# Kernel tuning notes

Hardware: AMD Instinct MI355X
Metric: run time of the kernel (lower is better)

## Reference

```python
import jax, jax.numpy as jnp
import numpy as np

B, STATE_DIM, REF_DIM, T, H, ACT_DIM = 2048, 32, 16, 100, 256, 2
IN_DIM = STATE_DIM + REF_DIM  # 48


def setup_inputs() -> dict:
    key = jax.random.key(0)
    ks = jax.random.split(key, 12)
    s = 1.0 / np.sqrt(H)  # PyTorch GRU init scale
    obs = jax.random.normal(ks[0], (B, STATE_DIM + T * REF_DIM), jnp.float32)
    u = lambda k, shape: jax.random.uniform(k, shape, jnp.float32, -s, s)
    return {
        "obs": obs,
        "w_ih_l0": u(ks[1], (3 * H, IN_DIM)),
        "w_hh_l0": u(ks[2], (3 * H, H)),
        "b_ih_l0": u(ks[3], (3 * H,)),
        "b_hh_l0": u(ks[4], (3 * H,)),
        "w_ih_l1": u(ks[5], (3 * H, H)),
        "w_hh_l1": u(ks[6], (3 * H, H)),
        "b_ih_l1": u(ks[7], (3 * H,)),
        "b_hh_l1": u(ks[8], (3 * H,)),
        "fc_w": u(ks[9], (ACT_DIM, H)),
        "fc_b": u(ks[10], (ACT_DIM,)),
        "act_high": jnp.ones((ACT_DIM,), jnp.float32),
        "act_low": -jnp.ones((ACT_DIM,), jnp.float32),
    }


def _gru_layer(x, w_ih, w_hh, b_ih, b_hh):
    # x: [B, T, D] -> outputs [B, T, H]; PyTorch GRU gate math (r, z, n order)
    h_dim = w_hh.shape[1]
    xg = jnp.einsum("btd,gd->btg", x, w_ih) + b_ih  # [B, T, 3H], precompute input gates

    def step(h, xg_t):
        hg = h @ w_hh.T + b_hh
        xr, xz, xn = jnp.split(xg_t, 3, axis=-1)
        hr, hz, hn = jnp.split(hg, 3, axis=-1)
        r = jax.nn.sigmoid(xr + hr)
        z = jax.nn.sigmoid(xz + hz)
        n = jnp.tanh(xn + r * hn)
        h_new = (1.0 - z) * n + z * h
        return h_new, h_new

    h0 = jnp.zeros((x.shape[0], h_dim), x.dtype)
    _, hs = jax.lax.scan(step, h0, jnp.swapaxes(xg, 0, 1))  # [T, B, H]
    return jnp.swapaxes(hs, 0, 1)


def reference(obs, w_ih_l0, w_hh_l0, b_ih_l0, b_hh_l0, w_ih_l1, w_hh_l1, b_ih_l1, b_hh_l1, fc_w, fc_b, act_high, act_low):
    state = obs[:, :STATE_DIM]                                  # [B, S]
    traj = obs[:, STATE_DIM:].reshape(obs.shape[0], -1, REF_DIM)  # [B, T, R]
    seq_len = traj.shape[1]
    state_exp = jnp.broadcast_to(state[:, None, :], (obs.shape[0], seq_len, STATE_DIM))
    x = jnp.concatenate([state_exp, traj], axis=2)              # [B, T, S+R]
    out = _gru_layer(x, w_ih_l0, w_hh_l0, b_ih_l0, b_hh_l0)
    out = _gru_layer(out, w_ih_l1, w_hh_l1, b_ih_l1, b_hh_l1)
    last = out[:, -1, :]                                        # [B, H]
    actions = last @ fc_w.T + fc_b                              # [B, A]
    return (act_high - act_low) / 2 * jnp.tanh(actions) + (act_high + act_low) / 2
```

## Files before the change

kernel.cpp:

```cpp
#include <hip/hip_runtime.h>
#include <hip/hip_bf16.h>
#include <stdint.h>
#include <stddef.h>


#define OBS_STRIDE 1632
#define H 256
#define M 16
#define THREADS 512

typedef __attribute__((ext_vector_type(8))) short bfrag8;
typedef __attribute__((ext_vector_type(4))) short bfrag4;
typedef __attribute__((ext_vector_type(4))) float floatx4;

#define MFMA16(a, b, c) __builtin_amdgcn_mfma_f32_16x16x32_bf16((a), (b), (c), 0, 0, 0)

__device__ __forceinline__ unsigned short f2bf(float f) {
  union { float f; unsigned int i; } v; v.f = f;
  unsigned int i = v.i + 0x7FFFu + ((v.i >> 16) & 1u);
  return (unsigned short)(i >> 16);
}
__device__ __forceinline__ float bf2f(unsigned short u) {
  union { unsigned int i; float f; } v; v.i = ((unsigned int)u) << 16; return v.f;
}
__device__ __forceinline__ float fsigm(float x) {
  return __builtin_amdgcn_rcpf(1.f + __builtin_amdgcn_exp2f(-1.44269504f * x));
}
__device__ __forceinline__ float ftanh(float x) {
  return 1.f - 2.f * __builtin_amdgcn_rcpf(1.f + __builtin_amdgcn_exp2f(2.88539008f * x));
}

__device__ __forceinline__ void ld16_async(bfrag8& d, const unsigned short* p) {
  asm volatile("global_load_dwordx4 %0, %1, off" : "=v"(d) : "v"(p));
}
__device__ __forceinline__ void wait6(bfrag8& a, bfrag8& b, bfrag8& c,
                                      bfrag8& d, bfrag8& e, bfrag8& f) {
  asm volatile("s_waitcnt vmcnt(0)"
               : "+v"(a), "+v"(b), "+v"(c), "+v"(d), "+v"(e), "+v"(f) :: "memory");
}
__device__ __forceinline__ void wait8_vm0(bfrag8& a, bfrag8& b, bfrag8& c, bfrag8& d,
                                          bfrag8& e, bfrag8& f, bfrag8& g, bfrag8& h) {
  asm volatile("s_waitcnt vmcnt(0)"
               : "+v"(a), "+v"(b), "+v"(c), "+v"(d),
                 "+v"(e), "+v"(f), "+v"(g), "+v"(h) :: "memory");
}
__device__ __forceinline__ void wait8_vm12(bfrag8& a, bfrag8& b, bfrag8& c, bfrag8& d,
                                           bfrag8& e, bfrag8& f, bfrag8& g, bfrag8& h) {
  asm volatile("s_waitcnt vmcnt(12)"
               : "+v"(a), "+v"(b), "+v"(c), "+v"(d),
                 "+v"(e), "+v"(f), "+v"(g), "+v"(h) :: "memory");
}
__device__ __forceinline__ void barrier_lgkm() {
  asm volatile("s_waitcnt lgkmcnt(0)\n\ts_barrier" ::: "memory");
}

__global__ void k_prep(const float* __restrict__ wih0, const float* __restrict__ whh0,
                       const float* __restrict__ wih1, const float* __restrict__ whh1,
                       unsigned short* __restrict__ o_wihs, unsigned short* __restrict__ o_wihr,
                       unsigned short* __restrict__ o_whh0,
                       unsigned short* __restrict__ o_wih1, unsigned short* __restrict__ o_whh1,
                       float* __restrict__ h0, float* __restrict__ h1) {
  long idx = (long)blockIdx.x * blockDim.x + threadIdx.x;
  const long ns = 768L * 32, n1 = 768L * 256, nh = 2048L * 256;
  if (idx < ns) { long r = idx >> 5, c = idx & 31;
                  o_wihs[idx] = f2bf(wih0[r * 48 + c]); return; }
  idx -= ns;
  if (idx < ns) { long r = idx >> 5, c = idx & 31;
                  o_wihr[idx] = (c < 16) ? f2bf(wih0[r * 48 + 32 + c]) : (unsigned short)0; return; }
  idx -= ns;
  if (idx < n1) { o_whh0[idx] = f2bf(whh0[idx]); return; }
  idx -= n1;
  if (idx < n1) { o_wih1[idx] = f2bf(wih1[idx]); return; }
  idx -= n1;
  if (idx < n1) { o_whh1[idx] = f2bf(whh1[idx]); return; }
  idx -= n1;
  if (idx < nh) { h0[idx] = 0.f; return; }
  idx -= nh;
  if (idx < nh) { h1[idx] = 0.f; return; }
}

__global__ __launch_bounds__(THREADS, 2) void k_fused(
    const float* __restrict__ obs,
    const unsigned short* __restrict__ g_wihs,
    const unsigned short* __restrict__ g_wihr,
    const unsigned short* __restrict__ g_whh0,
    const float* __restrict__ b_ih0, const float* __restrict__ b_hh0,
    float* __restrict__ h0state,
    unsigned short* __restrict__ out0c,
    const unsigned short* __restrict__ xg1c,
    const unsigned short* __restrict__ g_whh1,
    const float* __restrict__ b_ih1, const float* __restrict__ b_hh1,
    float* __restrict__ h1state,
    const float* __restrict__ fc_w, const float* __restrict__ fc_b,
    const float* __restrict__ act_high, const float* __restrict__ act_low,
    float* __restrict__ dout,
    int t0, int Tc, int do_l0, int do_l1, int is_last) {
  __shared__ __align__(16) unsigned short s_mem[71936];

  const int tid = threadIdx.x;
  const int wv = tid >> 6, lane = tid & 63, ln = lane & 15, qd = lane >> 4;
  const int role = blockIdx.x >> 7;
  const int bblk = blockIdx.x & 127;
  const int b0 = bblk * M;

  if (role == 0) {
    if (!do_l0) return;
    unsigned short* s_whh6 = s_mem;
    unsigned short* s_whh7 = s_mem + 30720;
    unsigned short* s_hA   = s_mem + 61440;
    unsigned short* s_x    = s_mem + 69888;
    unsigned short* s_st   = s_mem + 70912;

    for (int i = tid * 8; i < 768 * 32; i += THREADS * 8) {
      int m = i >> 5, c = i & 31;
      *(bfrag8*)&s_whh6[m * 40 + c] = *(const bfrag8*)&g_whh0[m * 256 + 192 + c];
      *(bfrag8*)&s_whh7[m * 40 + c] = *(const bfrag8*)&g_whh0[m * 256 + 224 + c];
    }
    { int r = tid >> 5, c = tid & 31;
      s_st[tid] = f2bf(obs[(size_t)(b0 + r) * OBS_STRIDE + c]); }
    if (tid < 256) {
      int r = tid >> 4, c = tid & 15;
      s_x[r * 32 + c] = f2bf(obs[(size_t)(b0 + r) * OBS_STRIDE + 32 + (size_t)t0 * 16 + c]);
      s_x[r * 32 + 16 + c] = 0;
      s_x[512 + r * 32 + 16 + c] = 0;
    }

    bfrag8 wf[6][6];
#pragma unroll
    for (int ks = 0; ks < 6; ++ks) {
#pragma unroll
      for (int f = 0; f < 6; ++f) {
        int nt = (f >> 1) * 16 + 2 * wv + (f & 1);
        ld16_async(wf[f][ks], g_whh0 + (size_t)(nt * 16 + ln) * 256 + ks * 32 + qd * 8);
      }
      wait6(wf[0][ks], wf[1][ks], wf[2][ks], wf[3][ks], wf[4][ks], wf[5][ks]);
    }
    bfrag8 wir[6];
#pragma unroll
    for (int f = 0; f < 6; ++f) {
      int nt = (f >> 1) * 16 + 2 * wv + (f & 1);
      wir[f] = *(const bfrag8*)&g_wihr[(size_t)(nt * 16 + ln) * 32 + qd * 8];
    }
    float bias_hn[2];
#pragma unroll
    for (int p = 0; p < 2; ++p) bias_hn[p] = b_hh0[512 + wv * 32 + p * 16 + ln];

    float h[2][4];
#pragma unroll
    for (int p = 0; p < 2; ++p)
#pragma unroll
      for (int i = 0; i < 4; ++i)
        h[p][i] = h0state[(size_t)(b0 + qd * 4 + i) * H + wv * 32 + p * 16 + ln];

    __syncthreads();

    floatx4 cc[6];
    {
      bfrag8 a_st = *(const bfrag8*)&s_st[ln * 32 + qd * 8];
#pragma unroll
      for (int f = 0; f < 6; ++f) {
        int nt = (f >> 1) * 16 + 2 * wv + (f & 1);
        int m = nt * 16 + ln;
        bfrag8 b_st = *(const bfrag8*)&g_wihs[(size_t)m * 32 + qd * 8];
        cc[f] = MFMA16(a_st, b_st, ((floatx4){0.f, 0.f, 0.f, 0.f}));
        float badd = b_ih0[m] + ((f < 4) ? b_hh0[m] : 0.f);
#pragma unroll
        for (int i = 0; i < 4; ++i) cc[f][i] += badd;
      }
    }
#pragma unroll
    for (int p = 0; p < 2; ++p)
#pragma unroll
      for (int i = 0; i < 4; ++i)
        s_hA[(qd * 4 + i) * 264 + wv * 32 + p * 16 + ln] = f2bf(h[p][i]);
    __syncthreads();

    const int orow = tid >> 5, ocol = (tid & 31) * 8;
    for (int tt = 0; tt < Tc; ++tt) {
      const int cur = tt & 1, nxt = cur ^ 1;
      if (tt > 0) {
        bfrag8 hv = *(const bfrag8*)&s_hA[cur * 4224 + orow * 264 + ocol];
        *(bfrag8*)&out0c[((size_t)(tt - 1) * 2048 + b0 + orow) * 256 + ocol] = hv;
      }
      float nref = 0.f;
      {
        int tl = (tt + 1 < Tc) ? tt + 1 : tt;
        if (tid < 256)
          nref = obs[(size_t)(b0 + (tid >> 4)) * OBS_STRIDE + 32 +
                     (size_t)(t0 + tl) * 16 + (tid & 15)];
      }

      floatx4 C[8];
#pragma unroll
      for (int f = 0; f < 6; ++f) C[f] = cc[f];
      C[6] = (floatx4){0.f, 0.f, 0.f, 0.f};
      C[7] = (floatx4){0.f, 0.f, 0.f, 0.f};

      {
        bfrag8 ax = *(const bfrag8*)&s_x[cur * 512 + ln * 32 + qd * 8];
        C[0] = MFMA16(ax, wir[0], C[0]);
        C[1] = MFMA16(ax, wir[1], C[1]);
        C[2] = MFMA16(ax, wir[2], C[2]);
        C[3] = MFMA16(ax, wir[3], C[3]);
        C[4] = MFMA16(ax, wir[4], C[4]);
        C[5] = MFMA16(ax, wir[5], C[5]);
      }
#pragma unroll
      for (int ks = 0; ks < 6; ++ks) {
        bfrag8 ah = *(const bfrag8*)&s_hA[cur * 4224 + ln * 264 + ks * 32 + qd * 8];
        C[0] = MFMA16(ah, wf[0][ks], C[0]);
        C[1] = MFMA16(ah, wf[1][ks], C[1]);
        C[2] = MFMA16(ah, wf[2][ks], C[2]);
        C[3] = MFMA16(ah, wf[3][ks], C[3]);
        C[6] = MFMA16(ah, wf[4][ks], C[6]);
        C[7] = MFMA16(ah, wf[5][ks], C[7]);
      }
      {
        bfrag8 ah = *(const bfrag8*)&s_hA[cur * 4224 + ln * 264 + 192 + qd * 8];
#pragma unroll
        for (int f = 0; f < 6; ++f) {
          int nt = (f >> 1) * 16 + 2 * wv + (f & 1);
          bfrag8 bh = *(const bfrag8*)&s_whh6[(nt * 16 + ln) * 40 + qd * 8];
          int ci = (f < 4) ? f : f + 2;
          C[ci] = MFMA16(ah, bh, C[ci]);
        }
      }
      {
        bfrag8 ah = *(const bfrag8*)&s_hA[cur * 4224 + ln * 264 + 224 + qd * 8];
#pragma unroll
        for (int f = 0; f < 6; ++f) {
          int nt = (f >> 1) * 16 + 2 * wv + (f & 1);
          bfrag8 bh = *(const bfrag8*)&s_whh7[(nt * 16 + ln) * 40 + qd * 8];
          int ci = (f < 4) ? f : f + 2;
          C[ci] = MFMA16(ah, bh, C[ci]);
        }
      }
#pragma unroll
      for (int p = 0; p < 2; ++p)
#pragma unroll
        for (int i = 0; i < 4; ++i) {
          float r = fsigm(C[0 + p][i]);
          float z = fsigm(C[2 + p][i]);
          float n = ftanh(C[4 + p][i] + r * (C[6 + p][i] + bias_hn[p]));
          h[p][i] = n + z * (h[p][i] - n);
          s_hA[nxt * 4224 + (qd * 4 + i) * 264 + wv * 32 + p * 16 + ln] = f2bf(h[p][i]);
        }
      if (tid < 256) s_x[nxt * 512 + (tid >> 4) * 32 + (tid & 15)] = f2bf(nref);
      barrier_lgkm();
    }
    {
      const int fb = Tc & 1;
      bfrag8 hv = *(const bfrag8*)&s_hA[fb * 4224 + orow * 264 + ocol];
      *(bfrag8*)&out0c[((size_t)(Tc - 1) * 2048 + b0 + orow) * 256 + ocol] = hv;
    }
#pragma unroll
    for (int p = 0; p < 2; ++p)
#pragma unroll
      for (int i = 0; i < 4; ++i)
        h0state[(size_t)(b0 + qd * 4 + i) * H + wv * 32 + p * 16 + ln] = h[p][i];

  } else {
    if (!do_l1) return;
    unsigned short* s_whh7 = s_mem;
    unsigned short* s_hA   = s_mem + 30720;

    for (int i = tid * 8; i < 768 * 32; i += THREADS * 8) {
      int m = i >> 5, c = i & 31;
      *(bfrag8*)&s_whh7[m * 40 + c] = *(const bfrag8*)&g_whh1[m * 256 + 224 + c];
    }
    bfrag8 wf[6][7];
#pragma unroll
    for (int ks = 0; ks < 7; ++ks) {
#pragma unroll
      for (int f = 0; f < 6; ++f) {
        int nt = (f >> 1) * 16 + 2 * wv + (f & 1);
        ld16_async(wf[f][ks], g_whh1 + (size_t)(nt * 16 + ln) * 256 + ks * 32 + qd * 8);
      }
      wait6(wf[0][ks], wf[1][ks], wf[2][ks], wf[3][ks], wf[4][ks], wf[5][ks]);
    }
    float bias_r[2], bias_z[2], bias_xn[2], bias_hn[2];
#pragma unroll
    for (int p = 0; p < 2; ++p) {
      int col = wv * 32 + p * 16 + ln;
      bias_r[p] = b_ih1[col] + b_hh1[col];
      bias_z[p] = b_ih1[256 + col] + b_hh1[256 + col];
      bias_xn[p] = b_ih1[512 + col];
      bias_hn[p] = b_hh1[512 + col];
    }
    float h[2][4];
#pragma unroll
    for (int p = 0; p < 2; ++p)
#pragma unroll
      for (int i = 0; i < 4; ++i)
        h[p][i] = h1state[(size_t)(b0 + qd * 4 + i) * H + wv * 32 + p * 16 + ln];
#pragma unroll
    for (int p = 0; p < 2; ++p)
#pragma unroll
      for (int i = 0; i < 4; ++i)
        s_hA[(qd * 4 + i) * 264 + wv * 32 + p * 16 + ln] = f2bf(h[p][i]);

    size_t offx[2][3];
#pragma unroll
    for (int p = 0; p < 2; ++p) {
      int col = wv * 32 + p * 16 + ln;
#pragma unroll
      for (int g = 0; g < 3; ++g)
        offx[p][g] = (size_t)(g * 256 + col) * 16 + qd * 4;
    }
    bfrag4 xr[2], xz[2], xn[2];
    {
      const unsigned short* xb = xg1c + (size_t)bblk * (768 * 16);
#pragma unroll
      for (int p = 0; p < 2; ++p) {
        xr[p] = *(const bfrag4*)&xb[offx[p][0]];
        xz[p] = *(const bfrag4*)&xb[offx[p][1]];
        xn[p] = *(const bfrag4*)&xb[offx[p][2]];
      }
    }
    __syncthreads();

    for (int tt = 0; tt < Tc; ++tt) {
      const int cur = tt & 1, nxt = cur ^ 1;
      bfrag4 nxr[2], nxz[2], nxn[2];
      {
        int tl = (tt + 1 < Tc) ? tt + 1 : tt;
        const unsigned short* xb = xg1c + ((size_t)tl * 128 + bblk) * (768 * 16);
#pragma unroll
        for (int p = 0; p < 2; ++p) {
          nxr[p] = *(const bfrag4*)&xb[offx[p][0]];
          nxz[p] = *(const bfrag4*)&xb[offx[p][1]];
          nxn[p] = *(const bfrag4*)&xb[offx[p][2]];
        }
      }

      floatx4 C[6];
#pragma unroll
      for (int i = 0; i < 6; ++i) C[i] = (floatx4){0.f, 0.f, 0.f, 0.f};
#pragma unroll
      for (int ks = 0; ks < 7; ++ks) {
        bfrag8 ah = *(const bfrag8*)&s_hA[cur * 4224 + ln * 264 + ks * 32 + qd * 8];
        C[0] = MFMA16(ah, wf[0][ks], C[0]);
        C[1] = MFMA16(ah, wf[1][ks], C[1]);
        C[2] = MFMA16(ah, wf[2][ks], C[2]);
        C[3] = MFMA16(ah, wf[3][ks], C[3]);
        C[4] = MFMA16(ah, wf[4][ks], C[4]);
        C[5] = MFMA16(ah, wf[5][ks], C[5]);
      }
      {
        bfrag8 ah = *(const bfrag8*)&s_hA[cur * 4224 + ln * 264 + 224 + qd * 8];
#pragma unroll
        for (int f = 0; f < 6; ++f) {
          int nt = (f >> 1) * 16 + 2 * wv + (f & 1);
          bfrag8 bh = *(const bfrag8*)&s_whh7[(nt * 16 + ln) * 40 + qd * 8];
          C[f] = MFMA16(ah, bh, C[f]);
        }
      }
#pragma unroll
      for (int p = 0; p < 2; ++p)
#pragma unroll
        for (int i = 0; i < 4; ++i) {
          float r = fsigm(C[0 + p][i] + bf2f((unsigned short)xr[p][i]) + bias_r[p]);
          float z = fsigm(C[2 + p][i] + bf2f((unsigned short)xz[p][i]) + bias_z[p]);
          float n = ftanh(bf2f((unsigned short)xn[p][i]) + bias_xn[p] +
                          r * (C[4 + p][i] + bias_hn[p]));
          h[p][i] = n + z * (h[p][i] - n);
          s_hA[nxt * 4224 + (qd * 4 + i) * 264 + wv * 32 + p * 16 + ln] = f2bf(h[p][i]);
        }
#pragma unroll
      for (int p = 0; p < 2; ++p) { xr[p] = nxr[p]; xz[p] = nxz[p]; xn[p] = nxn[p]; }
      barrier_lgkm();
    }
#pragma unroll
    for (int p = 0; p < 2; ++p)
#pragma unroll
      for (int i = 0; i < 4; ++i)
        h1state[(size_t)(b0 + qd * 4 + i) * H + wv * 32 + p * 16 + ln] = h[p][i];

    if (is_last) {
      const int fb = Tc & 1;
      int r = tid >> 5, a = (tid >> 4) & 1, kseg = tid & 15;
      float acc = 0.f;
#pragma unroll
      for (int j = 0; j < 16; ++j) {
        int k = kseg * 16 + j;
        acc += bf2f(s_hA[fb * 4224 + r * 264 + k]) * fc_w[a * H + k];
      }
      acc += __shfl_down(acc, 8);
      acc += __shfl_down(acc, 4);
      acc += __shfl_down(acc, 2);
      acc += __shfl_down(acc, 1);
      if (kseg == 0) {
        acc += fc_b[a];
        float hi = act_high[a], lo = act_low[a];
        float th = ftanh(acc);
        dout[(size_t)(b0 + r) * 2 + a] = 0.5f * (hi - lo) * th + 0.5f * (hi + lo);
      }
    }
  }
}

__global__ __launch_bounds__(THREADS, 2) void k_xg1(
    const unsigned short* __restrict__ out0c,
    const unsigned short* __restrict__ g_wih1,
    unsigned short* __restrict__ xg1c,
    int Tc) {
  const int tid = threadIdx.x;
  const int wv = tid >> 6, lane = tid & 63, ln = lane & 15, qd = lane >> 4;
  const int blk = blockIdx.x;
  const int tt = blk >> 5;
  const int bb = (blk >> 1) & 15;
  const int gh = blk & 1;

  bfrag8 af[3][8];
#pragma unroll
  for (int ks = 0; ks < 8; ++ks)
#pragma unroll
    for (int f = 0; f < 3; ++f) {
      int nt = gh * 24 + wv * 3 + f;
      ld16_async(af[f][ks], g_wih1 + (size_t)(nt * 16 + ln) * 256 + ks * 32 + qd * 8);
    }
  wait8_vm0(af[0][0], af[0][1], af[0][2], af[0][3], af[0][4], af[0][5], af[0][6], af[0][7]);
  wait8_vm0(af[1][0], af[1][1], af[1][2], af[1][3], af[1][4], af[1][5], af[1][6], af[1][7]);
  wait8_vm0(af[2][0], af[2][1], af[2][2], af[2][3], af[2][4], af[2][5], af[2][6], af[2][7]);

  const unsigned short* gsrc = out0c + ((size_t)tt * 2048 + bb * 128 + ln) * 256 + qd * 8;

  bfrag8 fr[2][8];
#pragma unroll
  for (int ks = 0; ks < 8; ++ks) ld16_async(fr[0][ks], gsrc + ks * 32);
  wait8_vm0(fr[0][0], fr[0][1], fr[0][2], fr[0][3], fr[0][4], fr[0][5], fr[0][6], fr[0][7]);

#pragma unroll
  for (int bt = 0; bt < 8; ++bt) {
    const int cur = bt & 1, nxt = cur ^ 1;
    if (bt < 7) {
      const unsigned short* nsrc = gsrc + (size_t)(bt + 1) * 16 * 256;
#pragma unroll
      for (int ks = 0; ks < 8; ++ks) ld16_async(fr[nxt][ks], nsrc + ks * 32);
    }
    floatx4 C[3];
#pragma unroll
    for (int f = 0; f < 3; ++f) C[f] = (floatx4){0.f, 0.f, 0.f, 0.f};
#pragma unroll
    for (int ks = 0; ks < 8; ++ks) {
      C[0] = MFMA16(af[0][ks], fr[cur][ks], C[0]);
      C[1] = MFMA16(af[1][ks], fr[cur][ks], C[1]);
      C[2] = MFMA16(af[2][ks], fr[cur][ks], C[2]);
    }
    const size_t obase = ((size_t)tt * 128 + bb * 8 + bt) * (768 * 16);
#pragma unroll
    for (int f = 0; f < 3; ++f) {
      int nt = gh * 24 + wv * 3 + f;
#pragma unroll
      for (int i = 0; i < 4; ++i) {
        int m = nt * 16 + qd * 4 + i;
        xg1c[obase + (size_t)m * 16 + ln] = f2bf(C[f][i]);
      }
    }
    if (bt < 7)
      wait8_vm12(fr[nxt][0], fr[nxt][1], fr[nxt][2], fr[nxt][3],
                 fr[nxt][4], fr[nxt][5], fr[nxt][6], fr[nxt][7]);
  }
}

extern "C" void kernel_launch(void* const* d_in, const int* in_sizes, int n_in,
                              void* d_out, int out_size, void* d_ws, size_t ws_size,
                              hipStream_t stream) {
  const float* obs  = (const float*)d_in[0];
  const float* wih0 = (const float*)d_in[1];
  const float* whh0 = (const float*)d_in[2];
  const float* bih0 = (const float*)d_in[3];
  const float* bhh0 = (const float*)d_in[4];
  const float* wih1 = (const float*)d_in[5];
  const float* whh1 = (const float*)d_in[6];
  const float* bih1 = (const float*)d_in[7];
  const float* bhh1 = (const float*)d_in[8];
  const float* fcw  = (const float*)d_in[9];
  const float* fcb  = (const float*)d_in[10];
  const float* ahigh= (const float*)d_in[11];
  const float* alow = (const float*)d_in[12];

  char* ws = (char*)d_ws;
  unsigned short* ws_wihs = (unsigned short*)(ws + 0);
  unsigned short* ws_wihr = (unsigned short*)(ws + 49152);
  unsigned short* ws_whh0 = (unsigned short*)(ws + 98304);
  unsigned short* ws_wih1 = (unsigned short*)(ws + 491520);
  unsigned short* ws_whh1 = (unsigned short*)(ws + 884736);
  float* h0 = (float*)(ws + 1277952);
  float* h1 = (float*)(ws + 3375104);
  const size_t base = 5472256;

  int Tc = 1;
  const int cands[7] = {25, 20, 10, 5, 4, 2, 1};
  for (int i = 0; i < 7; ++i) {
    size_t need = base + (size_t)4194304 * cands[i];
    if (need <= ws_size) { Tc = cands[i]; break; }
  }
  unsigned short* out0c = (unsigned short*)(ws + base);
  unsigned short* xg1c  = (unsigned short*)(ws + base + (size_t)1048576 * Tc);
  const int nc = 100 / Tc;

  const long total_prep = 2 * 768L * 32 + 3 * 768L * 256 + 2 * 2048L * 256;
  k_prep<<<(int)((total_prep + 255) / 256), 256, 0, stream>>>(
      wih0, whh0, wih1, whh1, ws_wihs, ws_wihr, ws_whh0, ws_wih1, ws_whh1, h0, h1);

  for (int c = 0; c <= nc; ++c) {
    k_fused<<<256, THREADS, 0, stream>>>(
        obs, ws_wihs, ws_wihr, ws_whh0, bih0, bhh0, h0, out0c,
        xg1c, ws_whh1, bih1, bhh1, h1, fcw, fcb, ahigh, alow, (float*)d_out,
        c * Tc, Tc, (c < nc) ? 1 : 0, (c > 0) ? 1 : 0, (c == nc) ? 1 : 0);
    if (c < nc)
      k_xg1<<<Tc * 32, THREADS, 0, stream>>>(out0c, ws_wih1, xg1c, Tc);
  }
}
```

Before: 797.4 us.

## Retile layer-1 input-gate GEMM so each block covers all batch rows per gate group

The k_xg1 kernel is re-partitioned. Each block now owns 4 gate tiles (64 gate rows) across the full 2048 batch, with each wave taking a 16-row slice per step over 16 steps, instead of each block owning 24 gate tiles for 128 batch rows. This cuts the grid from Tc*32 to Tc*12 blocks and lowers the number of times the weight fragments are reloaded per timestep. The vmcnt waits are moved before the MFMAs with larger outstanding counts to keep the next batch tile's loads in flight. In exchange, register pressure rises (4x8 weight fragments) and there are fewer blocks to fill the GPU.

```diff
diff --git a/kernel.cpp b/kernel.cpp
--- a/kernel.cpp
+++ b/kernel.cpp
@@ -44,9 +44,15 @@
                : "+v"(a), "+v"(b), "+v"(c), "+v"(d),
                  "+v"(e), "+v"(f), "+v"(g), "+v"(h) :: "memory");
 }
-__device__ __forceinline__ void wait8_vm12(bfrag8& a, bfrag8& b, bfrag8& c, bfrag8& d,
+__device__ __forceinline__ void wait8_vm24(bfrag8& a, bfrag8& b, bfrag8& c, bfrag8& d,
                                            bfrag8& e, bfrag8& f, bfrag8& g, bfrag8& h) {
-  asm volatile("s_waitcnt vmcnt(12)"
+  asm volatile("s_waitcnt vmcnt(24)"
+               : "+v"(a), "+v"(b), "+v"(c), "+v"(d),
+                 "+v"(e), "+v"(f), "+v"(g), "+v"(h) :: "memory");
+}
+__device__ __forceinline__ void wait8_vm16(bfrag8& a, bfrag8& b, bfrag8& c, bfrag8& d,
+                                           bfrag8& e, bfrag8& f, bfrag8& g, bfrag8& h) {
+  asm volatile("s_waitcnt vmcnt(16)"
                : "+v"(a), "+v"(b), "+v"(c), "+v"(d),
                  "+v"(e), "+v"(f), "+v"(g), "+v"(h) :: "memory");
 }
@@ -406,60 +412,69 @@
     int Tc) {
   const int tid = threadIdx.x;
   const int wv = tid >> 6, lane = tid & 63, ln = lane & 15, qd = lane >> 4;
-  const int blk = blockIdx.x;
-  const int tt = blk >> 5;
-  const int bb = (blk >> 1) & 15;
-  const int gh = blk & 1;
-
-  bfrag8 af[3][8];
+  const int tt = blockIdx.x / 12;
+  const int gg = blockIdx.x % 12;
+
+  bfrag8 af[4][8];
 #pragma unroll
   for (int ks = 0; ks < 8; ++ks)
 #pragma unroll
-    for (int f = 0; f < 3; ++f) {
-      int nt = gh * 24 + wv * 3 + f;
+    for (int f = 0; f < 4; ++f) {
+      int nt = gg * 4 + f;
       ld16_async(af[f][ks], g_wih1 + (size_t)(nt * 16 + ln) * 256 + ks * 32 + qd * 8);
     }
   wait8_vm0(af[0][0], af[0][1], af[0][2], af[0][3], af[0][4], af[0][5], af[0][6], af[0][7]);
   wait8_vm0(af[1][0], af[1][1], af[1][2], af[1][3], af[1][4], af[1][5], af[1][6], af[1][7]);
   wait8_vm0(af[2][0], af[2][1], af[2][2], af[2][3], af[2][4], af[2][5], af[2][6], af[2][7]);
-
-  const unsigned short* gsrc = out0c + ((size_t)tt * 2048 + bb * 128 + ln) * 256 + qd * 8;
+  wait8_vm0(af[3][0], af[3][1], af[3][2], af[3][3], af[3][4], af[3][5], af[3][6], af[3][7]);
+
+  const unsigned short* gsrc =
+      out0c + ((size_t)tt * 2048 + wv * 16 + ln) * 256 + qd * 8;
 
   bfrag8 fr[2][8];
 #pragma unroll
   for (int ks = 0; ks < 8; ++ks) ld16_async(fr[0][ks], gsrc + ks * 32);
-  wait8_vm0(fr[0][0], fr[0][1], fr[0][2], fr[0][3], fr[0][4], fr[0][5], fr[0][6], fr[0][7]);
-
-#pragma unroll
-  for (int bt = 0; bt < 8; ++bt) {
+
+#pragma unroll
+  for (int bt = 0; bt < 16; ++bt) {
     const int cur = bt & 1, nxt = cur ^ 1;
-    if (bt < 7) {
-      const unsigned short* nsrc = gsrc + (size_t)(bt + 1) * 16 * 256;
+    if (bt < 15) {
+      const unsigned short* nsrc = gsrc + (size_t)(bt + 1) * 128 * 256;
 #pragma unroll
       for (int ks = 0; ks < 8; ++ks) ld16_async(fr[nxt][ks], nsrc + ks * 32);
     }
-    floatx4 C[3];
-#pragma unroll
-    for (int f = 0; f < 3; ++f) C[f] = (floatx4){0.f, 0.f, 0.f, 0.f};
+    if (bt == 0) {
+      asm volatile("s_waitcnt vmcnt(8)"
+                   : "+v"(fr[0][0]), "+v"(fr[0][1]), "+v"(fr[0][2]), "+v"(fr[0][3]),
+                     "+v"(fr[0][4]), "+v"(fr[0][5]), "+v"(fr[0][6]), "+v"(fr[0][7])
+                   :: "memory");
+    } else if (bt < 15) {
+      wait8_vm24(fr[cur][0], fr[cur][1], fr[cur][2], fr[cur][3],
+                 fr[cur][4], fr[cur][5], fr[cur][6], fr[cur][7]);
+    } else {
+      wait8_vm16(fr[cur][0], fr[cur][1], fr[cur][2], fr[cur][3],
+                 fr[cur][4], fr[cur][5], fr[cur][6], fr[cur][7]);
+    }
+    floatx4 C[4];
+#pragma unroll
+    for (int f = 0; f < 4; ++f) C[f] = (floatx4){0.f, 0.f, 0.f, 0.f};
 #pragma unroll
     for (int ks = 0; ks < 8; ++ks) {
       C[0] = MFMA16(af[0][ks], fr[cur][ks], C[0]);
       C[1] = MFMA16(af[1][ks], fr[cur][ks], C[1]);
       C[2] = MFMA16(af[2][ks], fr[cur][ks], C[2]);
-    }
-    const size_t obase = ((size_t)tt * 128 + bb * 8 + bt) * (768 * 16);
-#pragma unroll
-    for (int f = 0; f < 3; ++f) {
-      int nt = gh * 24 + wv * 3 + f;
+      C[3] = MFMA16(af[3][ks], fr[cur][ks], C[3]);
+    }
+    const size_t obase = ((size_t)tt * 128 + bt * 8 + wv) * (768 * 16);
+#pragma unroll
+    for (int f = 0; f < 4; ++f) {
+      int nt = gg * 4 + f;
 #pragma unroll
       for (int i = 0; i < 4; ++i) {
         int m = nt * 16 + qd * 4 + i;
         xg1c[obase + (size_t)m * 16 + ln] = f2bf(C[f][i]);
       }
     }
-    if (bt < 7)
-      wait8_vm12(fr[nxt][0], fr[nxt][1], fr[nxt][2], fr[nxt][3],
-                 fr[nxt][4], fr[nxt][5], fr[nxt][6], fr[nxt][7]);
   }
 }
 
@@ -510,6 +525,6 @@
         xg1c, ws_whh1, bih1, bhh1, h1, fcw, fcb, ahigh, alow, (float*)d_out,
         c * Tc, Tc, (c < nc) ? 1 : 0, (c > 0) ? 1 : 0, (c == nc) ? 1 : 0);
     if (c < nc)
-      k_xg1<<<Tc * 32, THREADS, 0, stream>>>(out0c, ws_wih1, xg1c, Tc);
+      k_xg1<<<Tc * 12, THREADS, 0, stream>>>(out0c, ws_wih1, xg1c, Tc);
   }
 }
```

After: 793.0 us. About the same (-0.5%).
